# Optimization experiments

Hardware: AMD Instinct MI355X
Metric: run time of the kernel (lower is better)

The kernel has to match this reference:

```python
import jax, jax.numpy as jnp
import numpy as np

EPS = 1e-6

def _rms_norm(t):
    rms = jnp.sqrt(jnp.mean(t * t, axis=-1, keepdims=True) + EPS)
    return t / rms

def setup_inputs() -> dict:
    key = jax.random.key(0)
    ks = jax.random.split(key, 7)
    B, N, IN, OUT, R = 16, 2048, 256, 256, 64
    x = jax.random.normal(ks[0], (B, N, 4, IN), dtype=jnp.float32)
    # factors initialized as random normals (orthogonal init in torch; distribution irrelevant for math)
    scale = 1.0 / np.sqrt(IN)
    factor_tl = jax.random.normal(ks[1], (N, R, IN), dtype=jnp.float32) * scale
    factor_tr = jax.random.normal(ks[2], (N, R, IN), dtype=jnp.float32) * scale
    factor_bl = jax.random.normal(ks[3], (N, R, IN), dtype=jnp.float32) * scale
    factor_br = jax.random.normal(ks[4], (N, R, IN), dtype=jnp.float32) * scale
    factor_out = jax.random.normal(ks[5], (N, R, OUT), dtype=jnp.float32) * (1.0 / np.sqrt(R))
    gain = jnp.ones((N, 1), dtype=jnp.float32)
    return {"x": x, "factor_tl": factor_tl, "factor_tr": factor_tr,
            "factor_bl": factor_bl, "factor_br": factor_br,
            "factor_out": factor_out, "gain": gain}

def reference(x, factor_tl, factor_tr, factor_bl, factor_br, factor_out, gain):
    # per-node batched projections: [B,N,in] x [N,R,in] -> [B,N,R]
    p_tl = _rms_norm(jnp.einsum('bni,nri->bnr', x[:, :, 0, :], factor_tl))
    p_tr = _rms_norm(jnp.einsum('bni,nri->bnr', x[:, :, 1, :], factor_tr))
    p_bl = _rms_norm(jnp.einsum('bni,nri->bnr', x[:, :, 2, :], factor_bl))
    p_br = _rms_norm(jnp.einsum('bni,nri->bnr', x[:, :, 3, :], factor_br))
    merged = p_tl * p_tr * p_bl * p_br * gain[None, :, :]  # [B,N,R]
    out = jnp.einsum('bnr,nro->bno', merged, factor_out)   # [B,N,out]
    # use_residual=True, in_dim == out_dim -> identity residual projection
    return out + jnp.mean(x, axis=2)
```

## Files before the change

kernel.cpp:

```cpp
#include <hip/hip_runtime.h>
#include <math.h>


#define WAITVM(NLIT) asm volatile("s_waitcnt vmcnt(" #NLIT ")" ::: "memory")

__device__ __forceinline__ void g2l16(const float* g, float* l) {
  __builtin_amdgcn_global_load_lds(
      (const __attribute__((address_space(1))) void*)g,
      (__attribute__((address_space(3))) void*)l, 16, 0, 0);
}

#define NN 2048

__global__ __launch_bounds__(512, 2) void cpquad_kernel(
    const float* __restrict__ x,
    const float* __restrict__ ftl, const float* __restrict__ ftr,
    const float* __restrict__ fbl, const float* __restrict__ fbr,
    const float* __restrict__ fout, const float* __restrict__ gain,
    float* __restrict__ out) {

  alignas(16) __shared__ float s_st[8 * 2 * 768];
  __shared__ float s_ps[4096];
  __shared__ float s_rr[64];

  const int t = threadIdx.x, lane = t & 63, wid = t >> 6;
  const int n = blockIdx.x;
  const float gn = gain[n];

  const int iseg = t & 3;
  const int bh   = (t >> 2) & 1;
  const int rg   = (t >> 3) & 15;
  const int qq   = t >> 7;
  const int rh   = wid & 1;
  const int rj   = rg & 7;

  const float* fq0 = (qq == 0) ? ftl : ((qq == 1) ? ftr : ((qq == 2) ? fbl : fbr));

  const int rl = lane >> 2, c = lane & 3;
  const float* pA = fq0 + ((size_t)n * 64 + (rl >> 3) * 16 + rh * 8 + (rl & 7)) * 256 + c * 4;
  const float* pB = pA + 8192;
  const float* pX = x + (((size_t)rl * NN + n) * 4 + qq) * 256 + c * 4;

  float* wbase = s_st + wid * 1536;

  auto ISSUE = [&](int p) {
    float* d = wbase + (p & 1) * 768;
    g2l16(pA + p * 16, d);
    g2l16(pB + p * 16, d + 256);
    g2l16(pX + p * 16, d + 512);
  };

  ISSUE(0);

  float acc[4][8];
#pragma unroll
  for (int k = 0; k < 4; ++k)
#pragma unroll
    for (int b = 0; b < 8; ++b) acc[k][b] = 0.0f;

#pragma unroll 2
  for (int p = 0; p < 16; ++p) {
    if (p < 15) {
      ISSUE(p + 1);
      WAITVM(3);
    } else {
      WAITVM(0);
    }
    const float* sb = wbase + (p & 1) * 768;
    float4 fv[4];
#pragma unroll
    for (int k = 0; k < 4; ++k)
      fv[k] = *(const float4*)(sb + (k * 8 + rj) * 16 + iseg * 4);
#pragma unroll
    for (int h2 = 0; h2 < 2; ++h2) {
      float4 xv[4];
#pragma unroll
      for (int bb = 0; bb < 4; ++bb)
        xv[bb] = *(const float4*)(sb + 512 + (bh * 8 + h2 * 4 + bb) * 16 + iseg * 4);
#pragma unroll
      for (int k = 0; k < 4; ++k)
#pragma unroll
        for (int bb = 0; bb < 4; ++bb) {
          acc[k][h2 * 4 + bb] = fmaf(fv[k].x, xv[bb].x, acc[k][h2 * 4 + bb]);
          acc[k][h2 * 4 + bb] = fmaf(fv[k].y, xv[bb].y, acc[k][h2 * 4 + bb]);
          acc[k][h2 * 4 + bb] = fmaf(fv[k].z, xv[bb].z, acc[k][h2 * 4 + bb]);
          acc[k][h2 * 4 + bb] = fmaf(fv[k].w, xv[bb].w, acc[k][h2 * 4 + bb]);
        }
    }
  }

#pragma unroll
  for (int k = 0; k < 4; ++k)
#pragma unroll
    for (int b = 0; b < 8; ++b) {
      float v = acc[k][b];
      v += __shfl_xor(v, 1);
      v += __shfl_xor(v, 2);
      acc[k][b] = v;
    }
#pragma unroll
  for (int k = 0; k < 4; ++k) {
    if (iseg == k) {
#pragma unroll
      for (int b = 0; b < 8; ++b)
        s_ps[qq * 1024 + (bh * 8 + b) * 64 + k * 16 + rg] = acc[k][b];
    }
  }
  __syncthreads();

#pragma unroll
  for (int j = 0; j < 8; ++j) {
    const int row = wid * 8 + j;
    const float v = s_ps[row * 64 + lane];
    float ssum = v * v;
#pragma unroll
    for (int d = 1; d < 64; d <<= 1) ssum += __shfl_xor(ssum, d);
    if (lane == 0) s_rr[row] = 1.0f / sqrtf(ssum * (1.0f / 64.0f) + 1e-6f);
  }
  __syncthreads();

#pragma unroll
  for (int e0 = 0; e0 < 2; ++e0) {
    const int e = t + e0 * 512;
    const int b = e >> 6, r = e & 63;
    float m = gn;
#pragma unroll
    for (int q = 0; q < 4; ++q) m *= s_ps[q * 1024 + b * 64 + r] * s_rr[q * 16 + b];
    s_ps[b * 64 + r] = m;
  }
  __syncthreads();

  const float mv0 = s_ps[(wid * 2 + 0) * 64 + lane];
  const float mv1 = s_ps[(wid * 2 + 1) * 64 + lane];
  const float* fo_n = fout + (size_t)n * 16384 + (lane << 2);

  float oa[2][4] = {{0.f, 0.f, 0.f, 0.f}, {0.f, 0.f, 0.f, 0.f}};
#pragma unroll 8
  for (int rr = 0; rr < 64; ++rr) {
    const float4 f4 = *(const float4*)(fo_n + rr * 256);
    const float m0 = __uint_as_float(__builtin_amdgcn_readlane(__float_as_uint(mv0), rr));
    const float m1 = __uint_as_float(__builtin_amdgcn_readlane(__float_as_uint(mv1), rr));
    oa[0][0] = fmaf(m0, f4.x, oa[0][0]); oa[0][1] = fmaf(m0, f4.y, oa[0][1]);
    oa[0][2] = fmaf(m0, f4.z, oa[0][2]); oa[0][3] = fmaf(m0, f4.w, oa[0][3]);
    oa[1][0] = fmaf(m1, f4.x, oa[1][0]); oa[1][1] = fmaf(m1, f4.y, oa[1][1]);
    oa[1][2] = fmaf(m1, f4.z, oa[1][2]); oa[1][3] = fmaf(m1, f4.w, oa[1][3]);
  }

#pragma unroll
  for (int bb = 0; bb < 2; ++bb) {
    const int b = wid * 2 + bb;
    const float* xe = x + (((size_t)b * NN + n) * 4) * 256 + (lane << 2);
    float4 x0 = *(const float4*)(xe);
    float4 x1 = *(const float4*)(xe + 256);
    float4 x2 = *(const float4*)(xe + 512);
    float4 x3 = *(const float4*)(xe + 768);
    float4 o4;
    o4.x = oa[bb][0] + 0.25f * (x0.x + x1.x + x2.x + x3.x);
    o4.y = oa[bb][1] + 0.25f * (x0.y + x1.y + x2.y + x3.y);
    o4.z = oa[bb][2] + 0.25f * (x0.z + x1.z + x2.z + x3.z);
    o4.w = oa[bb][3] + 0.25f * (x0.w + x1.w + x2.w + x3.w);
    *(float4*)(out + ((size_t)b * NN + n) * 256 + (lane << 2)) = o4;
  }
}

extern "C" void kernel_launch(void* const* d_in, const int* in_sizes, int n_in,
                              void* d_out, int out_size, void* d_ws, size_t ws_size,
                              hipStream_t stream) {
  const float* x   = (const float*)d_in[0];
  const float* ftl = (const float*)d_in[1];
  const float* ftr = (const float*)d_in[2];
  const float* fbl = (const float*)d_in[3];
  const float* fbr = (const float*)d_in[4];
  const float* fo  = (const float*)d_in[5];
  const float* gn  = (const float*)d_in[6];
  float* o = (float*)d_out;
  cpquad_kernel<<<dim3(NN), dim3(512), 0, stream>>>(x, ftl, ftr, fbl, fbr, fo, gn, o);
}
```

Baseline: 215.2 us.

## Triple-buffer LDS staging with swizzled factor layout and aliased scratch

Replaces the double-buffered global-to-LDS staging with a triple-buffered pipeline that keeps two stages in flight, separating factor and x buffers per wave. Factor loads are XOR-swizzled in LDS to reduce bank conflicts on the float4 reads. The projection scratch now aliases the staging buffer, and the RMS normalisation is applied in place, which removes the separate reciprocal array. The larger per-wave staging buffer raises LDS use and adds an extra barrier plus an lgkmcnt wait each iteration, which could limit occupancy at two blocks per CU.

```diff
diff --git a/kernel.cpp b/kernel.cpp
--- a/kernel.cpp
+++ b/kernel.cpp
@@ -3,6 +3,8 @@
 
 
 #define WAITVM(NLIT) asm volatile("s_waitcnt vmcnt(" #NLIT ")" ::: "memory")
+#define LGKM0()      asm volatile("s_waitcnt lgkmcnt(0)" ::: "memory")
+#define MEMFENCE()   asm volatile("" ::: "memory")
 
 __device__ __forceinline__ void g2l16(const float* g, float* l) {
   __builtin_amdgcn_global_load_lds(
@@ -19,9 +21,8 @@
     const float* __restrict__ fout, const float* __restrict__ gain,
     float* __restrict__ out) {
 
-  alignas(16) __shared__ float s_st[8 * 2 * 768];
-  __shared__ float s_ps[4096];
-  __shared__ float s_rr[64];
+  alignas(16) __shared__ float s_st[8 * 2304];
+  float* s_ps = s_st;
 
   const int t = threadIdx.x, lane = t & 63, wid = t >> 6;
   const int n = blockIdx.x;
@@ -33,24 +34,32 @@
   const int qq   = t >> 7;
   const int rh   = wid & 1;
   const int rj   = rg & 7;
+  const int fsl  = (iseg ^ (rj & 3)) << 2;
 
   const float* fq0 = (qq == 0) ? ftl : ((qq == 1) ? ftr : ((qq == 2) ? fbl : fbr));
 
   const int rl = lane >> 2, c = lane & 3;
-  const float* pA = fq0 + ((size_t)n * 64 + (rl >> 3) * 16 + rh * 8 + (rl & 7)) * 256 + c * 4;
+  const float* pA = fq0 + ((size_t)n * 64 + (rl >> 3) * 16 + rh * 8 + (rl & 7)) * 256
+                        + ((c ^ (rl & 3)) << 2);
   const float* pB = pA + 8192;
-  const float* pX = x + (((size_t)rl * NN + n) * 4 + qq) * 256 + c * 4;
+  const float* pX = x + (((size_t)rl * NN + n) * 4 + qq) * 256 + (c << 2);
 
-  float* wbase = s_st + wid * 1536;
+  float* wf = s_st + wid * 2304;
+  float* wx = wf + 1536;
 
-  auto ISSUE = [&](int p) {
-    float* d = wbase + (p & 1) * 768;
-    g2l16(pA + p * 16, d);
-    g2l16(pB + p * 16, d + 256);
-    g2l16(pX + p * 16, d + 512);
+  auto ISSUE_F = [&](int s) {
+    float* d = wf + (s % 3) * 512;
+    g2l16(pA + s * 16, d);
+    g2l16(pB + s * 16, d + 256);
+  };
+  auto ISSUE_X = [&](int s) {
+    g2l16(pX + s * 16, wx + (s % 3) * 256);
   };
 
-  ISSUE(0);
+  ISSUE_F(0); ISSUE_X(0);
+  MEMFENCE();
+  ISSUE_F(1); ISSUE_X(1);
+  MEMFENCE();
 
   float acc[4][8];
 #pragma unroll
@@ -60,23 +69,27 @@
 
 #pragma unroll 2
   for (int p = 0; p < 16; ++p) {
-    if (p < 15) {
-      ISSUE(p + 1);
+    if (p < 14) {
+      ISSUE_F(p + 2);
+      ISSUE_X(p + 2);
+      WAITVM(6);
+    } else if (p == 14) {
       WAITVM(3);
     } else {
       WAITVM(0);
     }
-    const float* sb = wbase + (p & 1) * 768;
+    const float* sb = wf + (p % 3) * 512;
+    const float* xb = wx + (p % 3) * 256;
     float4 fv[4];
 #pragma unroll
     for (int k = 0; k < 4; ++k)
-      fv[k] = *(const float4*)(sb + (k * 8 + rj) * 16 + iseg * 4);
+      fv[k] = *(const float4*)(sb + (k * 8 + rj) * 16 + fsl);
 #pragma unroll
     for (int h2 = 0; h2 < 2; ++h2) {
       float4 xv[4];
 #pragma unroll
       for (int bb = 0; bb < 4; ++bb)
-        xv[bb] = *(const float4*)(sb + 512 + (bh * 8 + h2 * 4 + bb) * 16 + iseg * 4);
+        xv[bb] = *(const float4*)(xb + (bh * 8 + h2 * 4 + bb) * 16 + iseg * 4);
 #pragma unroll
       for (int k = 0; k < 4; ++k)
 #pragma unroll
@@ -87,6 +100,7 @@
           acc[k][h2 * 4 + bb] = fmaf(fv[k].w, xv[bb].w, acc[k][h2 * 4 + bb]);
         }
     }
+    LGKM0();
   }
 
 #pragma unroll
@@ -98,6 +112,7 @@
       v += __shfl_xor(v, 2);
       acc[k][b] = v;
     }
+  __syncthreads();
 #pragma unroll
   for (int k = 0; k < 4; ++k) {
     if (iseg == k) {
@@ -111,11 +126,12 @@
 #pragma unroll
   for (int j = 0; j < 8; ++j) {
     const int row = wid * 8 + j;
-    const float v = s_ps[row * 64 + lane];
+    float v = s_ps[row * 64 + lane];
     float ssum = v * v;
 #pragma unroll
     for (int d = 1; d < 64; d <<= 1) ssum += __shfl_xor(ssum, d);
-    if (lane == 0) s_rr[row] = 1.0f / sqrtf(ssum * (1.0f / 64.0f) + 1e-6f);
+    v *= 1.0f / sqrtf(ssum * (1.0f / 64.0f) + 1e-6f);
+    s_ps[row * 64 + lane] = v;
   }
   __syncthreads();
 
@@ -125,7 +141,7 @@
     const int b = e >> 6, r = e & 63;
     float m = gn;
 #pragma unroll
-    for (int q = 0; q < 4; ++q) m *= s_ps[q * 1024 + b * 64 + r] * s_rr[q * 16 + b];
+    for (int q = 0; q < 4; ++q) m *= s_ps[q * 1024 + b * 64 + r];
     s_ps[b * 64 + r] = m;
   }
   __syncthreads();
```

Result: no change. 212.9 us (-1.1%).
